# Optimization experiments

Hardware: AMD Instinct MI355X
Metric: run time of the kernel (lower is better)

## Reference

```python
import math
import jax, jax.numpy as jnp
import numpy as np

B, S, D, P, MAX_LEN = 32, 8192, 256, 64, 8192


def _sinusoid_table(max_len, d_model):
    pos = jnp.arange(max_len, dtype=jnp.float32)[:, None]
    div = jnp.exp(jnp.arange(0, d_model, 2, dtype=jnp.float32) * (-math.log(10000.0) / d_model))
    return jnp.stack([jnp.sin(pos * div), jnp.cos(pos * div)], axis=-1).reshape(max_len, d_model)


def setup_inputs() -> dict:
    key = jax.random.key(0)
    k1, k2, k3 = jax.random.split(key, 3)
    x = jax.random.normal(k1, (B, S, 1), dtype=jnp.float32)
    r_peak_indices = jnp.sort(jax.random.randint(k2, (B, P), 0, S), axis=1)
    n_peaks = jax.random.randint(k3, (B,), 8, P + 1)  # at least 8 valid peaks per sample
    pe = _sinusoid_table(MAX_LEN, D)  # registered buffer of the module
    return {"x": x, "pe": pe, "r_peak_indices": r_peak_indices, "n_peaks": n_peaks}


def reference(x, pe, r_peak_indices, n_peaks):
    batch, seq_len, _ = x.shape
    d_model = pe.shape[-1]
    max_len = pe.shape[0]
    pos = jnp.arange(seq_len, dtype=jnp.float32)  # [S]
    div_term = jnp.exp(jnp.arange(0, d_model, 2, dtype=jnp.float32) * (-math.log(10000.0) / d_model))

    def per_sample(peaks, n):  # peaks: [P] int, n: scalar int (valid count)
        peaks_f = peaks.astype(jnp.float32)
        valid = jnp.arange(peaks.shape[0]) < n  # [P]
        # nearest valid R peak per position
        dist = jnp.abs(pos[:, None] - peaks_f[None, :])  # [S, P]
        dist = jnp.where(valid[None, :], dist, jnp.inf)
        ni = jnp.argmin(dist, axis=1)  # [S]
        # rr_intervals: diff(peaks) with first interval duplicated at index 0
        diffs = peaks_f[1:] - peaks_f[:-1]  # [P-1]
        rr = jnp.concatenate([diffs[:1], diffs])  # [P]
        rr = jnp.where(n == 1, jnp.float32(max_len // 2), rr)
        avg_rr = jnp.maximum(1.0, jnp.sum(jnp.where(valid, rr, 0.0)) / n.astype(jnp.float32))
        nearest_pos = peaks_f[ni]
        nearest_rr = jnp.maximum(rr[ni], 1.0)
        rel = (pos - nearest_pos) / nearest_rr
        phase = jnp.abs(rel) % 1.0
        # interleaved sin/cos over cardiac phase
        enc = jnp.stack([jnp.sin(phase[:, None] * div_term),
                         jnp.cos(phase[:, None] * div_term)], axis=-1).reshape(seq_len, d_model)
        # special channels (d_model >= 8)
        is_peak = jnp.any((pos[:, None] == peaks_f[None, :]) & valid[None, :], axis=1)
        norm_rr = jnp.clip(nearest_rr / avg_rr, 0.5, 2.0)
        prev_rr = rr[jnp.maximum(ni - 1, 0)]
        hrv = jnp.where(ni > 0, jnp.minimum(jnp.abs(nearest_rr - prev_rr) / avg_rr, 1.0), 0.0)
        specials = jnp.stack([
            jnp.sin(rel * math.pi), jnp.cos(rel * math.pi),
            jnp.sin(phase * 2.0 * math.pi), jnp.cos(phase * 2.0 * math.pi),
            jnp.minimum(jnp.abs(pos - nearest_pos) / nearest_rr, 1.0),
            is_peak.astype(jnp.float32), norm_rr, hrv], axis=1)
        enc = enc.at[:, :8].set(specials)
        return jnp.where(n > 0, enc, pe[:seq_len])  # empty-peak fallback

    return jax.vmap(per_sample)(r_peak_indices, n_peaks)
```

## Files before the change

kernel.cpp:

```cpp
#include <hip/hip_runtime.h>
#include <math.h>

#define NB 32
#define NS 8192
#define ND 256
#define NP 64
#define TILE 256

#define DIV_C (-0.035977892f)
#define INV2PI 0.15915494f

typedef float vf4 __attribute__((ext_vector_type(4)));

__global__ __launch_bounds__(256) void rwave_pe_kernel(
    const float* __restrict__ pe,
    const int*   __restrict__ peaks,
    const int*   __restrict__ npk,
    float*       __restrict__ out)
{
    const int b    = blockIdx.y;
    const int tile = blockIdx.x;
    const int tid  = threadIdx.x;

    __shared__ float s_pk[NP];
    __shared__ float s_rr[NP];
    __shared__ float s_scal[TILE][9];

    const int n = npk[b];

    if (tid < NP) s_pk[tid] = (float)peaks[b * NP + tid];
    __syncthreads();
    if (tid < NP) {
        float rrv;
        if (n == 1)        rrv = 4096.0f;
        else if (tid == 0) rrv = s_pk[1] - s_pk[0];
        else               rrv = s_pk[tid] - s_pk[tid - 1];
        s_rr[tid] = rrv;
    }
    __syncthreads();

    if (n > 0) {
        const float posf = (float)(tile * TILE + tid);
        int   best  = 0;
        float bestd = INFINITY;
        float rrsum = 0.0f;
        bool  ispk  = false;
        for (int p = 0; p < n; ++p) {
            float d = fabsf(posf - s_pk[p]);
            if (d < bestd) { bestd = d; best = p; }
            ispk = ispk || (d == 0.0f);
            rrsum += s_rr[p];
        }
        const float avg   = fmaxf(1.0f, rrsum / (float)n);
        const float nrr   = fmaxf(s_rr[best], 1.0f);
        const float npos  = s_pk[best];
        const float rel   = (posf - npos) / nrr;
        const float arel  = fabsf(rel);
        const float phase = arel - floorf(arel);
        const float prevrr = s_rr[best > 0 ? best - 1 : 0];

        float th = rel * 0.5f;
        th = th - floorf(th);
        s_scal[tid][0] = __builtin_amdgcn_sinf(th);
        s_scal[tid][1] = __builtin_amdgcn_cosf(th);
        s_scal[tid][2] = __builtin_amdgcn_sinf(phase);
        s_scal[tid][3] = __builtin_amdgcn_cosf(phase);
        s_scal[tid][4] = fminf(arel, 1.0f);
        s_scal[tid][5] = ispk ? 1.0f : 0.0f;
        s_scal[tid][6] = fminf(fmaxf(nrr / avg, 0.5f), 2.0f);
        s_scal[tid][7] = (best > 0) ? fminf(fabsf(nrr - prevrr) / avg, 1.0f) : 0.0f;
        s_scal[tid][8] = phase;
    }
    __syncthreads();

    const int lane = tid & 63;
    const int wid  = tid >> 6;

    const float dv0 = expf((float)(4 * lane)     * DIV_C) * INV2PI;
    const float dv1 = expf((float)(4 * lane + 2) * DIV_C) * INV2PI;

    const size_t rowBase = (size_t)b * NS + (size_t)tile * TILE;
    vf4* outv = reinterpret_cast<vf4*>(out);

    for (int pl = wid; pl < TILE; pl += 4) {
        vf4 v;
        if (n > 0) {
            const float ph = s_scal[pl][8];
            const float t0 = ph * dv0;
            const float t1 = ph * dv1;
            v.x = __builtin_amdgcn_sinf(t0);
            v.y = __builtin_amdgcn_cosf(t0);
            v.z = __builtin_amdgcn_sinf(t1);
            v.w = __builtin_amdgcn_cosf(t1);
            if (lane < 2) {
                const int base = 4 * lane;
                v.x = s_scal[pl][base + 0];
                v.y = s_scal[pl][base + 1];
                v.z = s_scal[pl][base + 2];
                v.w = s_scal[pl][base + 3];
            }
        } else {
            const vf4* pev = reinterpret_cast<const vf4*>(pe);
            v = pev[((size_t)tile * TILE + (size_t)pl) * (ND / 4) + lane];
        }
        outv[(rowBase + (size_t)pl) * (ND / 4) + lane] = v;
    }
}

extern "C" void kernel_launch(void* const* d_in, const int* in_sizes, int n_in,
                              void* d_out, int out_size, void* d_ws, size_t ws_size,
                              hipStream_t stream) {
    (void)in_sizes; (void)n_in; (void)d_ws; (void)ws_size; (void)out_size;
    const float* pe    = (const float*)d_in[1];
    const int*   peaks = (const int*)d_in[2];
    const int*   npk   = (const int*)d_in[3];
    float*       out   = (float*)d_out;

    dim3 grid(NS / TILE, NB);
    rwave_pe_kernel<<<grid, 256, 0, stream>>>(pe, peaks, npk, out);
}
```

Baseline: 47.05 us.

## Replace shared-memory per-position scan with wavefront-parallel argmin via shuffles

Drops the shared-memory staging and the serial per-thread loop over peaks. Each lane now holds one peak, and for every output row the nearest peak is found with a packed (distance, index) xor-shuffle min reduction across the wavefront; rr and its average also come from shuffles. This removes the __syncthreads barriers and the O(n) serial loop, but adds six shuffles plus several lane broadcasts per row, all of it redundant work inside a kernel that is mostly bound by output writes.

```diff
diff --git a/kernel.cpp b/kernel.cpp
--- a/kernel.cpp
+++ b/kernel.cpp
@@ -21,60 +21,21 @@
     const int b    = blockIdx.y;
     const int tile = blockIdx.x;
     const int tid  = threadIdx.x;
-
-    __shared__ float s_pk[NP];
-    __shared__ float s_rr[NP];
-    __shared__ float s_scal[TILE][9];
+    const int lane = tid & 63;
+    const int wid  = tid >> 6;
 
     const int n = npk[b];
 
-    if (tid < NP) s_pk[tid] = (float)peaks[b * NP + tid];
-    __syncthreads();
-    if (tid < NP) {
-        float rrv;
-        if (n == 1)        rrv = 4096.0f;
-        else if (tid == 0) rrv = s_pk[1] - s_pk[0];
-        else               rrv = s_pk[tid] - s_pk[tid - 1];
-        s_rr[tid] = rrv;
-    }
-    __syncthreads();
-
-    if (n > 0) {
-        const float posf = (float)(tile * TILE + tid);
-        int   best  = 0;
-        float bestd = INFINITY;
-        float rrsum = 0.0f;
-        bool  ispk  = false;
-        for (int p = 0; p < n; ++p) {
-            float d = fabsf(posf - s_pk[p]);
-            if (d < bestd) { bestd = d; best = p; }
-            ispk = ispk || (d == 0.0f);
-            rrsum += s_rr[p];
-        }
-        const float avg   = fmaxf(1.0f, rrsum / (float)n);
-        const float nrr   = fmaxf(s_rr[best], 1.0f);
-        const float npos  = s_pk[best];
-        const float rel   = (posf - npos) / nrr;
-        const float arel  = fabsf(rel);
-        const float phase = arel - floorf(arel);
-        const float prevrr = s_rr[best > 0 ? best - 1 : 0];
-
-        float th = rel * 0.5f;
-        th = th - floorf(th);
-        s_scal[tid][0] = __builtin_amdgcn_sinf(th);
-        s_scal[tid][1] = __builtin_amdgcn_cosf(th);
-        s_scal[tid][2] = __builtin_amdgcn_sinf(phase);
-        s_scal[tid][3] = __builtin_amdgcn_cosf(phase);
-        s_scal[tid][4] = fminf(arel, 1.0f);
-        s_scal[tid][5] = ispk ? 1.0f : 0.0f;
-        s_scal[tid][6] = fminf(fmaxf(nrr / avg, 0.5f), 2.0f);
-        s_scal[tid][7] = (best > 0) ? fminf(fabsf(nrr - prevrr) / avg, 1.0f) : 0.0f;
-        s_scal[tid][8] = phase;
-    }
-    __syncthreads();
-
-    const int lane = tid & 63;
-    const int wid  = tid >> 6;
+    const int   ipk = peaks[b * NP + lane];
+    const float pk  = (float)ipk;
+    const float pk_prev = __shfl_up(pk, 1);
+    const float pk_next = __shfl_down(pk, 1);
+    float rr = (lane == 0) ? (pk_next - pk) : (pk - pk_prev);
+    if (n == 1) rr = 4096.0f;
+    float rrsum = (lane < n) ? rr : 0.0f;
+    #pragma unroll
+    for (int m = 1; m < 64; m <<= 1) rrsum += __shfl_xor(rrsum, m);
+    const float avg = fmaxf(1.0f, rrsum / (float)n);
 
     const float dv0 = expf((float)(4 * lane)     * DIV_C) * INV2PI;
     const float dv1 = expf((float)(4 * lane + 2) * DIV_C) * INV2PI;
@@ -82,28 +43,58 @@
     const size_t rowBase = (size_t)b * NS + (size_t)tile * TILE;
     vf4* outv = reinterpret_cast<vf4*>(out);
 
-    for (int pl = wid; pl < TILE; pl += 4) {
-        vf4 v;
-        if (n > 0) {
-            const float ph = s_scal[pl][8];
-            const float t0 = ph * dv0;
-            const float t1 = ph * dv1;
+    if (n > 0) {
+        for (int pl = wid; pl < TILE; pl += 4) {
+            const int pos = tile * TILE + pl;
+            const int idist = abs(pos - ipk);
+            int k = (lane < n) ? ((idist << 6) | lane) : 0x7FFFFFFF;
+            k = min(k, __shfl_xor(k, 1));
+            k = min(k, __shfl_xor(k, 2));
+            k = min(k, __shfl_xor(k, 4));
+            k = min(k, __shfl_xor(k, 8));
+            k = min(k, __shfl_xor(k, 16));
+            k = min(k, __shfl_xor(k, 32));
+            const int  best = k & 63;
+            const bool ispk = (k >> 6) == 0;
+
+            const float npos   = __shfl(pk, best);
+            const float nrr0   = __shfl(rr, best);
+            const float prevrr = __shfl(rr, best > 0 ? best - 1 : 0);
+            const float nrr    = fmaxf(nrr0, 1.0f);
+            const float rel    = ((float)pos - npos) / nrr;
+            const float arel   = fabsf(rel);
+            const float phase  = arel - floorf(arel);
+
+            vf4 v;
+            const float t0 = phase * dv0;
+            const float t1 = phase * dv1;
             v.x = __builtin_amdgcn_sinf(t0);
             v.y = __builtin_amdgcn_cosf(t0);
             v.z = __builtin_amdgcn_sinf(t1);
             v.w = __builtin_amdgcn_cosf(t1);
             if (lane < 2) {
-                const int base = 4 * lane;
-                v.x = s_scal[pl][base + 0];
-                v.y = s_scal[pl][base + 1];
-                v.z = s_scal[pl][base + 2];
-                v.w = s_scal[pl][base + 3];
+                if (lane == 0) {
+                    float th = rel * 0.5f;
+                    th = th - floorf(th);
+                    v.x = __builtin_amdgcn_sinf(th);
+                    v.y = __builtin_amdgcn_cosf(th);
+                    v.z = __builtin_amdgcn_sinf(phase);
+                    v.w = __builtin_amdgcn_cosf(phase);
+                } else {
+                    v.x = fminf(arel, 1.0f);
+                    v.y = ispk ? 1.0f : 0.0f;
+                    v.z = fminf(fmaxf(nrr / avg, 0.5f), 2.0f);
+                    v.w = (best > 0) ? fminf(fabsf(nrr - prevrr) / avg, 1.0f) : 0.0f;
+                }
             }
-        } else {
-            const vf4* pev = reinterpret_cast<const vf4*>(pe);
-            v = pev[((size_t)tile * TILE + (size_t)pl) * (ND / 4) + lane];
+            outv[(rowBase + (size_t)pl) * (ND / 4) + lane] = v;
         }
-        outv[(rowBase + (size_t)pl) * (ND / 4) + lane] = v;
+    } else {
+        const vf4* pev = reinterpret_cast<const vf4*>(pe);
+        for (int pl = wid; pl < TILE; pl += 4) {
+            vf4 v = pev[((size_t)tile * TILE + (size_t)pl) * (ND / 4) + lane];
+            outv[(rowBase + (size_t)pl) * (ND / 4) + lane] = v;
+        }
     }
 }
 
```

Measured after the change: 54.95 us. 1.17x slower.
